# Kernel optimization log

Hardware: AMD Instinct MI355X
Metric: run time of the kernel (lower is better)

The kernel has to match this reference:

```python
import jax, jax.numpy as jnp
import numpy as np

DIM = 768
HEADS = 12
HD = DIM // HEADS
SCALE = HD ** -0.5


def setup_inputs() -> dict:
    key = jax.random.key(0)
    ks = jax.random.split(key, 12)
    B, N = 2, 2048
    s = DIM ** -0.5
    return {
        "x1": jax.random.normal(ks[0], (B, N, DIM), jnp.float32),
        "x2": jax.random.normal(ks[1], (B, N, DIM), jnp.float32),
        "Wq": jax.random.normal(ks[2], (DIM, DIM), jnp.float32) * s,
        "bq": jax.random.normal(ks[3], (DIM,), jnp.float32) * 0.01,
        "Wk": jax.random.normal(ks[4], (DIM, DIM), jnp.float32) * s,
        "bk": jax.random.normal(ks[5], (DIM,), jnp.float32) * 0.01,
        "Wv": jax.random.normal(ks[6], (DIM, DIM), jnp.float32) * s,
        "bv": jax.random.normal(ks[7], (DIM,), jnp.float32) * 0.01,
        "Wo": jax.random.normal(ks[8], (DIM, DIM), jnp.float32) * s,
        "bo": jax.random.normal(ks[9], (DIM,), jnp.float32) * 0.01,
        "cross_scale": jnp.array([0.5], jnp.float32),
    }


def _heads(x, W, b):
    # torch Linear: x @ W.T + b; then (B,N,H,hd) -> (B,H,N,hd)
    B, N, _ = x.shape
    y = x @ W.T + b
    return y.reshape(B, N, HEADS, HD).transpose(0, 2, 1, 3)


def reference(x1, x2, Wq, bq, Wk, bk, Wv, bv, Wo, bo, cross_scale):
    B, N, C = x1.shape
    q1, k1, v1 = _heads(x1, Wq, bq), _heads(x1, Wk, bk), _heads(x1, Wv, bv)
    q2, k2, v2 = _heads(x2, Wq, bq), _heads(x2, Wk, bk), _heads(x2, Wv, bv)

    s = cross_scale[0]
    attn11 = jnp.einsum('bhqd,bhkd->bhqk', q1, k1) * SCALE
    attn22 = jnp.einsum('bhqd,bhkd->bhqk', q2, k2) * SCALE
    attn12 = jnp.einsum('bhqd,bhkd->bhqk', q1, k2) * SCALE
    attn21 = jnp.einsum('bhqd,bhkd->bhqk', q2, k1) * SCALE

    a1 = jax.nn.softmax((1.0 - s) * attn11 + s * attn12, axis=-1)
    a2 = jax.nn.softmax((1.0 - s) * attn22 + s * attn21, axis=-1)

    o1 = jnp.einsum('bhqk,bhkd->bhqd', a1, v1).transpose(0, 2, 1, 3).reshape(B, N, C)
    o2 = jnp.einsum('bhqk,bhkd->bhqd', a2, v2).transpose(0, 2, 1, 3).reshape(B, N, C)

    out1 = o1 @ Wo.T + bo
    out2 = o2 @ Wo.T + bo
    return out1, out2
```

## Files before the change

kernel.cpp:

```cpp
#include <hip/hip_runtime.h>

#define KDIM 768
#define HALF 3145728
#define XAELEMS 6291456
#define WELEMS 589824
#define QS 0.18033688f

typedef __attribute__((ext_vector_type(8))) short short8;
typedef __attribute__((ext_vector_type(4))) short short4_;
typedef __attribute__((ext_vector_type(4))) float float4_;
typedef __attribute__((ext_vector_type(2))) unsigned int uint2_;

__device__ __forceinline__ unsigned short f2bf(float f) {
  unsigned int u = __float_as_uint(f);
  u += 0x7fffu + ((u >> 16) & 1u);
  return (unsigned short)(u >> 16);
}

__device__ __forceinline__ unsigned int pack2bf(float a, float b) {
  unsigned int ua = __float_as_uint(a) + 0x8000u;
  unsigned int ub = __float_as_uint(b) + 0x8000u;
  return __builtin_amdgcn_perm(ub, ua, 0x07060302);
}

__device__ __forceinline__ void gll16(const void* g, void* l) {
  __builtin_amdgcn_global_load_lds(
      (const __attribute__((address_space(1))) unsigned int*)g,
      (__attribute__((address_space(3))) unsigned int*)l, 16, 0, 0);
}

__global__ void prep_x_kernel(const float* __restrict__ x1, const float* __restrict__ x2,
                              const float* __restrict__ cs,
                              unsigned short* __restrict__ xa, unsigned short* __restrict__ xb) {
  const int i = (blockIdx.x * 256 + threadIdx.x) * 4;
  const float s = cs[0], t_ = 1.0f - s;
  float4 a = *(const float4*)(x1 + i);
  float4 b = *(const float4*)(x2 + i);
  ushort4 ua = { f2bf(a.x), f2bf(a.y), f2bf(a.z), f2bf(a.w) };
  ushort4 ub = { f2bf(b.x), f2bf(b.y), f2bf(b.z), f2bf(b.w) };
  *(ushort4*)(xa + i) = ua;
  *(ushort4*)(xa + HALF + i) = ub;
  ushort4 c1 = { f2bf(t_*a.x + s*b.x), f2bf(t_*a.y + s*b.y), f2bf(t_*a.z + s*b.z), f2bf(t_*a.w + s*b.w) };
  ushort4 c2 = { f2bf(t_*b.x + s*a.x), f2bf(t_*b.y + s*a.y), f2bf(t_*b.z + s*a.z), f2bf(t_*b.w + s*a.w) };
  *(ushort4*)(xb + i) = c1;
  *(ushort4*)(xb + HALF + i) = c2;
}

__global__ void conv_w4_kernel(const float* __restrict__ w0, const float* __restrict__ w1,
                               const float* __restrict__ w2, const float* __restrict__ w3,
                               unsigned short* __restrict__ o0, unsigned short* __restrict__ o1,
                               unsigned short* __restrict__ o2, unsigned short* __restrict__ o3) {
  const int z = blockIdx.y;
  const float* w = (z == 0) ? w0 : (z == 1) ? w1 : (z == 2) ? w2 : w3;
  unsigned short* o = (z == 0) ? o0 : (z == 1) ? o1 : (z == 2) ? o2 : o3;
  const int i = (blockIdx.x * 256 + threadIdx.x) * 4;
  float4 a = *(const float4*)(w + i);
  ushort4 ua = { f2bf(a.x), f2bf(a.y), f2bf(a.z), f2bf(a.w) };
  *(ushort4*)(o + i) = ua;
}

__device__ __forceinline__ void gemm_mainloop(const unsigned short* __restrict__ A,
                                              const unsigned short* __restrict__ W,
                                              unsigned short* As, unsigned short* Bs,
                                              int m0, int n0, int t, float4_ (&acc)[4][4]) {
  const int lane = t & 63, quad = lane >> 4, lrow = lane & 15;
  const int wave = t >> 6;
  const int wm = (wave & 1) * 64, wn = (wave >> 1) * 64;
  for (int kt = 0; kt < KDIM; kt += 64) {
#pragma unroll
    for (int i = 0; i < 4; i++) {
      const int li = i * 256 + t;
      const int row = li >> 3, cc = (li & 7) * 8;
      gll16(A + (size_t)(m0 + row) * KDIM + kt + cc, As + li * 8);
      gll16(W + (size_t)(n0 + row) * KDIM + kt + cc, Bs + li * 8);
    }
    __syncthreads();
#pragma unroll
    for (int kk = 0; kk < 2; kk++) {
      short8 af[4], bfr[4];
#pragma unroll
      for (int i = 0; i < 4; i++)
        af[i] = *(const short8*)(As + (wm + i * 16 + lrow) * 64 + kk * 32 + quad * 8);
#pragma unroll
      for (int j = 0; j < 4; j++)
        bfr[j] = *(const short8*)(Bs + (wn + j * 16 + lrow) * 64 + kk * 32 + quad * 8);
#pragma unroll
      for (int i = 0; i < 4; i++)
#pragma unroll
        for (int j = 0; j < 4; j++)
          acc[i][j] = __builtin_amdgcn_mfma_f32_16x16x32_bf16(af[i], bfr[j], acc[i][j], 0, 0, 0);
    }
    __syncthreads();
  }
}

__global__ __launch_bounds__(256, 2)
void qkv_gemm(const unsigned short* __restrict__ xa, const unsigned short* __restrict__ xb,
              const unsigned short* __restrict__ wq, const unsigned short* __restrict__ wk,
              const unsigned short* __restrict__ wv,
              const float* __restrict__ bq, const float* __restrict__ bk, const float* __restrict__ bv,
              unsigned short* __restrict__ qo, unsigned short* __restrict__ ko,
              unsigned short* __restrict__ vto) {
  __shared__ __align__(16) unsigned short smem[16384];
  unsigned short* As = smem;
  unsigned short* Bs = smem + 8192;
  const int t = threadIdx.x;
  const int z = blockIdx.z;
  const int m0 = blockIdx.x * 128, n0 = blockIdx.y * 128;
  const unsigned short* A = (z == 1) ? xb : xa;
  const unsigned short* W = (z == 0) ? wq : (z == 1) ? wk : wv;
  const float* bias = (z == 0) ? bq : (z == 1) ? bk : bv;
  float4_ acc[4][4];
#pragma unroll
  for (int i = 0; i < 4; i++)
#pragma unroll
    for (int j = 0; j < 4; j++) acc[i][j] = (float4_){0.f, 0.f, 0.f, 0.f};
  gemm_mainloop(A, W, As, Bs, m0, n0, t, acc);

  const int lane = t & 63, quad = lane >> 4, lrow = lane & 15;
  const int wave = t >> 6;
  const int wm = (wave & 1) * 64, wn = (wave >> 1) * 64;

  if (z == 2) {
    unsigned short* Tb = smem + wave * 4096;
#pragma unroll
    for (int i = 0; i < 4; i++) {
#pragma unroll
      for (int j = 0; j < 4; j++) {
        const int nl = j * 16 + lrow;
        const float bn = bias[n0 + wn + nl];
#pragma unroll
        for (int r = 0; r < 4; r++) {
          const int ml = i * 16 + quad * 4 + r;
          const int c = ml >> 3;
          Tb[nl * 64 + ((c ^ (nl & 7)) * 8) + (ml & 7)] = f2bf(acc[i][j][r] + bn);
        }
      }
    }
    __asm__ __volatile__("s_waitcnt lgkmcnt(0)");
    const int sb = (m0 + wm) >> 11;
    const int hh = (n0 + wn) >> 6;
    const int tokbase = ((m0 + wm) & 2047);
#pragma unroll
    for (int i3 = 0; i3 < 8; i3++) {
      const int ci = i3 * 64 + lane;
      const int row = ci >> 3, p = ci & 7;
      short8 rd = *(const short8*)(Tb + row * 64 + p * 8);
      const int c = p ^ (row & 7);
      *(short8*)(vto + ((size_t)(sb * 12 + hh) * 64 + row) * 2048 + tokbase + c * 8) = rd;
    }
  } else {
    unsigned short* dst = (z == 0) ? qo : ko;
    const float scale = (z == 0) ? QS : 1.0f;
#pragma unroll
    for (int i = 0; i < 4; i++) {
#pragma unroll
      for (int j = 0; j < 4; j++) {
        const int n = n0 + wn + j * 16 + lrow;
        const float bn = bias[n];
#pragma unroll
        for (int r = 0; r < 4; r++) {
          const int m = m0 + wm + i * 16 + quad * 4 + r;
          dst[(size_t)m * KDIM + n] = f2bf((acc[i][j][r] + bn) * scale);
        }
      }
    }
  }
}

__global__ __launch_bounds__(256, 2)
void out_gemm(const unsigned short* __restrict__ ob, const unsigned short* __restrict__ wo,
              const float* __restrict__ bo, float* __restrict__ out) {
  __shared__ __align__(16) unsigned short As[128 * 64];
  __shared__ __align__(16) unsigned short Bs[128 * 64];
  const int t = threadIdx.x;
  const int m0 = blockIdx.x * 128, n0 = blockIdx.y * 128;
  float4_ acc[4][4];
#pragma unroll
  for (int i = 0; i < 4; i++)
#pragma unroll
    for (int j = 0; j < 4; j++) acc[i][j] = (float4_){0.f, 0.f, 0.f, 0.f};
  gemm_mainloop(ob, wo, As, Bs, m0, n0, t, acc);

  const int lane = t & 63, quad = lane >> 4, lrow = lane & 15;
  const int wave = t >> 6;
  const int wm = (wave & 1) * 64, wn = (wave >> 1) * 64;
#pragma unroll
  for (int i = 0; i < 4; i++) {
#pragma unroll
    for (int j = 0; j < 4; j++) {
      const int n = n0 + wn + j * 16 + lrow;
      const float bn = bo[n];
#pragma unroll
      for (int r = 0; r < 4; r++) {
        const int m = m0 + wm + i * 16 + quad * 4 + r;
        out[(size_t)m * KDIM + n] = acc[i][j][r] + bn;
      }
    }
  }
}

__global__ __launch_bounds__(256, 2)
void attn_kernel(const unsigned short* __restrict__ qg, const unsigned short* __restrict__ kg,
                 const unsigned short* __restrict__ vt, unsigned short* __restrict__ o) {
  __shared__ __align__(16) unsigned short Ks[3][64 * 64];
  __shared__ __align__(16) unsigned short Vs[3][64 * 64];
  const int prob = blockIdx.x % 48;
  const int q0 = (blockIdx.x / 48) * 128;
  const int sb = prob / 12, h = prob % 12;
  const int t = threadIdx.x, w = t >> 6, lane = t & 63, quad = lane >> 4, lrow = lane & 15;
  const int mbase = sb * 2048;
  const size_t vbase = (size_t)prob * (64 * 2048);

  short8 bq[2][2];
#pragma unroll
  for (int i = 0; i < 2; i++) {
    const unsigned short* qp = qg + (size_t)(mbase + q0 + w * 32 + i * 16 + lrow) * KDIM + h * 64 + quad * 8;
    bq[i][0] = *(const short8*)qp;
    bq[i][1] = *(const short8*)(qp + 32);
  }
  float l_part[2] = {0.f, 0.f};
  float4_ oa[2][4];
#pragma unroll
  for (int i = 0; i < 2; i++)
#pragma unroll
    for (int d = 0; d < 4; d++) oa[i][d] = (float4_){0.f, 0.f, 0.f, 0.f};

  auto stage = [&](int k0, int b) {
#pragma unroll
    for (int i2 = 0; i2 < 2; i2++) {
      const int li = i2 * 256 + t;
      const int row = li >> 3, p = li & 7;
      const int c = p ^ (row & 7);
      gll16(kg + (size_t)(mbase + k0 + row) * KDIM + h * 64 + c * 8, &Ks[b][li * 8]);
    }
#pragma unroll
    for (int i2 = 0; i2 < 2; i2++) {
      const int li = i2 * 256 + t;
      const int row = li >> 3, p = li & 7;
      const int c = p ^ (row & 7);
      gll16(vt + vbase + (size_t)row * 2048 + k0 + c * 8, &Vs[b][li * 8]);
    }
  };

  auto compute = [&](int b) {
    float4_ st[4][2];
#pragma unroll
    for (int nt = 0; nt < 4; nt++)
#pragma unroll
      for (int i = 0; i < 2; i++) st[nt][i] = (float4_){0.f, 0.f, 0.f, 0.f};
#pragma unroll
    for (int kk = 0; kk < 2; kk++) {
#pragma unroll
      for (int nt = 0; nt < 4; nt++) {
        short8 ak = *(const short8*)(&Ks[b][(nt * 16 + lrow) * 64 + (((kk * 4 + quad) ^ (lrow & 7)) * 8)]);
        st[nt][0] = __builtin_amdgcn_mfma_f32_16x16x32_bf16(ak, bq[0][kk], st[nt][0], 0, 0, 0);
        st[nt][1] = __builtin_amdgcn_mfma_f32_16x16x32_bf16(ak, bq[1][kk], st[nt][1], 0, 0, 0);
      }
    }

    short4_ pb[2][4];
#pragma unroll
    for (int nt = 0; nt < 4; nt++)
#pragma unroll
      for (int i = 0; i < 2; i++) {
        const float p0 = __builtin_amdgcn_exp2f(st[nt][i][0]);
        const float p1 = __builtin_amdgcn_exp2f(st[nt][i][1]);
        const float p2 = __builtin_amdgcn_exp2f(st[nt][i][2]);
        const float p3 = __builtin_amdgcn_exp2f(st[nt][i][3]);
        l_part[i] += (p0 + p1) + (p2 + p3);
        uint2_ uu = { pack2bf(p0, p1), pack2bf(p2, p3) };
        pb[i][nt] = __builtin_bit_cast(short4_, uu);
      }

#pragma unroll
    for (int g = 0; g < 2; g++) {
      const int cp0 = (((g * 4 + (quad >> 1)) ^ (lrow & 7)) * 8) + (quad & 1) * 4;
      const int cp1 = (((g * 4 + 2 + (quad >> 1)) ^ (lrow & 7)) * 8) + (quad & 1) * 4;
      const short8 b80 = __builtin_shufflevector(pb[0][2 * g], pb[0][2 * g + 1], 0, 1, 2, 3, 4, 5, 6, 7);
      const short8 b81 = __builtin_shufflevector(pb[1][2 * g], pb[1][2 * g + 1], 0, 1, 2, 3, 4, 5, 6, 7);
#pragma unroll
      for (int dt = 0; dt < 4; dt++) {
        const int rb = (dt * 16 + lrow) * 64;
        short4_ av0 = *(const short4_*)(&Vs[b][rb + cp0]);
        short4_ av1 = *(const short4_*)(&Vs[b][rb + cp1]);
        short8 a8 = __builtin_shufflevector(av0, av1, 0, 1, 2, 3, 4, 5, 6, 7);
        oa[0][dt] = __builtin_amdgcn_mfma_f32_16x16x32_bf16(a8, b80, oa[0][dt], 0, 0, 0);
        oa[1][dt] = __builtin_amdgcn_mfma_f32_16x16x32_bf16(a8, b81, oa[1][dt], 0, 0, 0);
      }
    }
  };

  stage(0, 0);
  stage(64, 1);

#define STEP(KT, CUR, STG)                                   \
  do {                                                       \
    asm volatile("s_waitcnt vmcnt(4)" ::: "memory");         \
    __builtin_amdgcn_s_barrier();                            \
    __builtin_amdgcn_sched_barrier(0);                       \
    stage(((KT) + 2) * 64, (STG));                           \
    compute(CUR);                                            \
  } while (0)

  for (int kt0 = 0; kt0 < 30; kt0 += 3) {
    STEP(kt0, 0, 2);
    STEP(kt0 + 1, 1, 0);
    STEP(kt0 + 2, 2, 1);
  }
  asm volatile("s_waitcnt vmcnt(4)" ::: "memory");
  __builtin_amdgcn_s_barrier();
  __builtin_amdgcn_sched_barrier(0);
  compute(0);
  asm volatile("s_waitcnt vmcnt(0)" ::: "memory");
  __builtin_amdgcn_s_barrier();
  __builtin_amdgcn_sched_barrier(0);
  compute(1);
#undef STEP

#pragma unroll
  for (int i = 0; i < 2; i++) {
    float l = l_part[i];
    l += __shfl_xor(l, 16);
    l += __shfl_xor(l, 32);
    const float inv = 1.0f / l;
    const size_t m = (size_t)mbase + q0 + w * 32 + i * 16 + lrow;
#pragma unroll
    for (int dt = 0; dt < 4; dt++) {
      uint2_ uu = { pack2bf(oa[i][dt][0] * inv, oa[i][dt][1] * inv),
                    pack2bf(oa[i][dt][2] * inv, oa[i][dt][3] * inv) };
      *(uint2_*)(o + m * KDIM + h * 64 + dt * 16 + quad * 4) = uu;
    }
  }
}

extern "C" void kernel_launch(void* const* d_in, const int* in_sizes, int n_in,
                              void* d_out, int out_size, void* d_ws, size_t ws_size,
                              hipStream_t stream) {
  const float* x1 = (const float*)d_in[0];
  const float* x2 = (const float*)d_in[1];
  const float* Wq = (const float*)d_in[2];
  const float* bq = (const float*)d_in[3];
  const float* Wk = (const float*)d_in[4];
  const float* bk = (const float*)d_in[5];
  const float* Wv = (const float*)d_in[6];
  const float* bv = (const float*)d_in[7];
  const float* Wo = (const float*)d_in[8];
  const float* bo = (const float*)d_in[9];
  const float* cs = (const float*)d_in[10];
  float* out = (float*)d_out;

  char* ws = (char*)d_ws;
  size_t off = 0;
  auto alloc = [&](size_t bytes) {
    void* p = ws + off;
    off += (bytes + 255) & ~(size_t)255;
    return p;
  };
  unsigned short* xa  = (unsigned short*)alloc((size_t)XAELEMS * 2);
  unsigned short* xb  = (unsigned short*)alloc((size_t)XAELEMS * 2);
  unsigned short* wqb = (unsigned short*)alloc((size_t)WELEMS * 2);
  unsigned short* wkb = (unsigned short*)alloc((size_t)WELEMS * 2);
  unsigned short* wvb = (unsigned short*)alloc((size_t)WELEMS * 2);
  unsigned short* wob = (unsigned short*)alloc((size_t)WELEMS * 2);
  unsigned short* qg  = (unsigned short*)alloc((size_t)XAELEMS * 2);
  unsigned short* kgb = (unsigned short*)alloc((size_t)XAELEMS * 2);
  unsigned short* vtb = (unsigned short*)alloc((size_t)XAELEMS * 2);
  unsigned short* ob  = (unsigned short*)alloc((size_t)XAELEMS * 2);

  prep_x_kernel<<<HALF / 1024, 256, 0, stream>>>(x1, x2, cs, xa, xb);
  conv_w4_kernel<<<dim3(WELEMS / 1024, 4), 256, 0, stream>>>(Wq, Wk, Wv, Wo, wqb, wkb, wvb, wob);
  qkv_gemm<<<dim3(64, 6, 3), 256, 0, stream>>>(xa, xb, wqb, wkb, wvb, bq, bk, bv, qg, kgb, vtb);
  attn_kernel<<<48 * 16, 256, 0, stream>>>(qg, kgb, vtb, ob);
  out_gemm<<<dim3(64, 6), 256, 0, stream>>>(ob, wob, bo, out);
}
```

Measured before the change: 224.2 us.

## Compute softmax row sums via MFMA with ones and pre-permute V layout

The attention kernel now gets the softmax denominator from an extra MFMA against an all-ones bf16 vector instead of scalar adds plus cross-lane shuffles. It also switches P to truncating bf16 packing, which keeps the numerator and the MFMA-computed denominator consistent. The V-transpose writer in the projection kernel now stores tokens pre-permuted, so the attention loop can read one 16-byte LDS vector instead of two 8-byte reads and a shuffle. The cost is two extra MFMAs per group in exchange for fewer VALU ops and LDS instructions, and the epilogue now does two half-width LDS reads.

Result: faster. 215.6 us (-3.8%).

```diff
diff --git a/kernel.cpp b/kernel.cpp
--- a/kernel.cpp
+++ b/kernel.cpp
@@ -21,6 +21,10 @@
   unsigned int ua = __float_as_uint(a) + 0x8000u;
   unsigned int ub = __float_as_uint(b) + 0x8000u;
   return __builtin_amdgcn_perm(ub, ua, 0x07060302);
+}
+
+__device__ __forceinline__ unsigned int pack2bf_t(float a, float b) {
+  return __builtin_amdgcn_perm(__float_as_uint(b), __float_as_uint(a), 0x07060302);
 }
 
 __device__ __forceinline__ void gll16(const void* g, void* l) {
@@ -144,10 +148,15 @@
 #pragma unroll
     for (int i3 = 0; i3 < 8; i3++) {
       const int ci = i3 * 64 + lane;
-      const int row = ci >> 3, p = ci & 7;
-      short8 rd = *(const short8*)(Tb + row * 64 + p * 8);
-      const int c = p ^ (row & 7);
-      *(short8*)(vto + ((size_t)(sb * 12 + hh) * 64 + row) * 2048 + tokbase + c * 8) = rd;
+      const int row = ci >> 3, cp_ = ci & 7;
+      const int bl = (cp_ >> 2) * 4 + ((cp_ & 3) >> 1);
+      const int off = (cp_ & 1) * 4;
+      const int chlo = bl ^ (row & 7);
+      const int chhi = (bl + 2) ^ (row & 7);
+      short4_ lo = *(const short4_*)(Tb + row * 64 + chlo * 8 + off);
+      short4_ hi = *(const short4_*)(Tb + row * 64 + chhi * 8 + off);
+      short8 rd = __builtin_shufflevector(lo, hi, 0, 1, 2, 3, 4, 5, 6, 7);
+      *(short8*)(vto + ((size_t)(sb * 12 + hh) * 64 + row) * 2048 + tokbase + cp_ * 8) = rd;
     }
   } else {
     unsigned short* dst = (z == 0) ? qo : ko;
@@ -212,6 +221,10 @@
   const int mbase = sb * 2048;
   const size_t vbase = (size_t)prob * (64 * 2048);
 
+  short8 ones8;
+#pragma unroll
+  for (int zz = 0; zz < 8; zz++) ones8[zz] = (short)0x3F80;
+
   short8 bq[2][2];
 #pragma unroll
   for (int i = 0; i < 2; i++) {
@@ -219,12 +232,14 @@
     bq[i][0] = *(const short8*)qp;
     bq[i][1] = *(const short8*)(qp + 32);
   }
-  float l_part[2] = {0.f, 0.f};
+  float4_ la[2];
   float4_ oa[2][4];
 #pragma unroll
-  for (int i = 0; i < 2; i++)
+  for (int i = 0; i < 2; i++) {
+    la[i] = (float4_){0.f, 0.f, 0.f, 0.f};
 #pragma unroll
     for (int d = 0; d < 4; d++) oa[i][d] = (float4_){0.f, 0.f, 0.f, 0.f};
+  }
 
   auto stage = [&](int k0, int b) {
 #pragma unroll
@@ -268,23 +283,20 @@
         const float p1 = __builtin_amdgcn_exp2f(st[nt][i][1]);
         const float p2 = __builtin_amdgcn_exp2f(st[nt][i][2]);
         const float p3 = __builtin_amdgcn_exp2f(st[nt][i][3]);
-        l_part[i] += (p0 + p1) + (p2 + p3);
-        uint2_ uu = { pack2bf(p0, p1), pack2bf(p2, p3) };
+        uint2_ uu = { pack2bf_t(p0, p1), pack2bf_t(p2, p3) };
         pb[i][nt] = __builtin_bit_cast(short4_, uu);
       }
 
 #pragma unroll
     for (int g = 0; g < 2; g++) {
-      const int cp0 = (((g * 4 + (quad >> 1)) ^ (lrow & 7)) * 8) + (quad & 1) * 4;
-      const int cp1 = (((g * 4 + 2 + (quad >> 1)) ^ (lrow & 7)) * 8) + (quad & 1) * 4;
       const short8 b80 = __builtin_shufflevector(pb[0][2 * g], pb[0][2 * g + 1], 0, 1, 2, 3, 4, 5, 6, 7);
       const short8 b81 = __builtin_shufflevector(pb[1][2 * g], pb[1][2 * g + 1], 0, 1, 2, 3, 4, 5, 6, 7);
+      la[0] = __builtin_amdgcn_mfma_f32_16x16x32_bf16(ones8, b80, la[0], 0, 0, 0);
+      la[1] = __builtin_amdgcn_mfma_f32_16x16x32_bf16(ones8, b81, la[1], 0, 0, 0);
 #pragma unroll
       for (int dt = 0; dt < 4; dt++) {
-        const int rb = (dt * 16 + lrow) * 64;
-        short4_ av0 = *(const short4_*)(&Vs[b][rb + cp0]);
-        short4_ av1 = *(const short4_*)(&Vs[b][rb + cp1]);
-        short8 a8 = __builtin_shufflevector(av0, av1, 0, 1, 2, 3, 4, 5, 6, 7);
+        const int rb = (dt * 16 + lrow) * 64 + (((g * 4 + quad) ^ (lrow & 7)) * 8);
+        short8 a8 = *(const short8*)(&Vs[b][rb]);
         oa[0][dt] = __builtin_amdgcn_mfma_f32_16x16x32_bf16(a8, b80, oa[0][dt], 0, 0, 0);
         oa[1][dt] = __builtin_amdgcn_mfma_f32_16x16x32_bf16(a8, b81, oa[1][dt], 0, 0, 0);
       }
@@ -320,10 +332,7 @@
 
 #pragma unroll
   for (int i = 0; i < 2; i++) {
-    float l = l_part[i];
-    l += __shfl_xor(l, 16);
-    l += __shfl_xor(l, 32);
-    const float inv = 1.0f / l;
+    const float inv = 1.0f / la[i][0];
     const size_t m = (size_t)mbase + q0 + w * 32 + i * 16 + lrow;
 #pragma unroll
     for (int dt = 0; dt < 4; dt++) {
```

## Pre-permute V^T token layout so attention loads V with single 16-byte reads

Applied to the files above, without the earlier changes.

The projection kernel now writes V^T with token columns permuted, so each lane's eight P·V operands are contiguous. The attention kernel can then fetch V fragments with one 16-byte LDS read instead of two 8-byte reads and a shuffle. The QK^T loop is also reordered to interleave each tile's exp/pack with the next tile's MFMAs, and to defer the last tile's exp past the first P·V group, so MFMA and VALU work overlap. This relies on the producer and consumer permutations matching exactly; the projection store now needs two 8-byte LDS reads per chunk.

Result: slower. 235.5 us (+5.1%).

```diff
diff --git a/kernel.cpp b/kernel.cpp
--- a/kernel.cpp
+++ b/kernel.cpp
@@ -144,10 +144,15 @@
 #pragma unroll
     for (int i3 = 0; i3 < 8; i3++) {
       const int ci = i3 * 64 + lane;
-      const int row = ci >> 3, p = ci & 7;
-      short8 rd = *(const short8*)(Tb + row * 64 + p * 8);
-      const int c = p ^ (row & 7);
-      *(short8*)(vto + ((size_t)(sb * 12 + hh) * 64 + row) * 2048 + tokbase + c * 8) = rd;
+      const int row = ci >> 3, cp_ = ci & 7;
+      const int bl = (cp_ >> 2) * 4 + ((cp_ & 3) >> 1);
+      const int off = (cp_ & 1) * 4;
+      const int chlo = bl ^ (row & 7);
+      const int chhi = (bl + 2) ^ (row & 7);
+      short4_ lo = *(const short4_*)(Tb + row * 64 + chlo * 8 + off);
+      short4_ hi = *(const short4_*)(Tb + row * 64 + chhi * 8 + off);
+      short8 rd = __builtin_shufflevector(lo, hi, 0, 1, 2, 3, 4, 5, 6, 7);
+      *(short8*)(vto + ((size_t)(sb * 12 + hh) * 64 + row) * 2048 + tokbase + cp_ * 8) = rd;
     }
   } else {
     unsigned short* dst = (z == 0) ? qo : ko;
@@ -212,6 +217,8 @@
   const int mbase = sb * 2048;
   const size_t vbase = (size_t)prob * (64 * 2048);
 
+  const float4_ z4 = (float4_){0.f, 0.f, 0.f, 0.f};
+
   short8 bq[2][2];
 #pragma unroll
   for (int i = 0; i < 2; i++) {
@@ -245,49 +252,45 @@
 
   auto compute = [&](int b) {
     float4_ st[4][2];
-#pragma unroll
-    for (int nt = 0; nt < 4; nt++)
-#pragma unroll
-      for (int i = 0; i < 2; i++) st[nt][i] = (float4_){0.f, 0.f, 0.f, 0.f};
-#pragma unroll
-    for (int kk = 0; kk < 2; kk++) {
-#pragma unroll
-      for (int nt = 0; nt < 4; nt++) {
-        short8 ak = *(const short8*)(&Ks[b][(nt * 16 + lrow) * 64 + (((kk * 4 + quad) ^ (lrow & 7)) * 8)]);
-        st[nt][0] = __builtin_amdgcn_mfma_f32_16x16x32_bf16(ak, bq[0][kk], st[nt][0], 0, 0, 0);
-        st[nt][1] = __builtin_amdgcn_mfma_f32_16x16x32_bf16(ak, bq[1][kk], st[nt][1], 0, 0, 0);
-      }
-    }
-
     short4_ pb[2][4];
-#pragma unroll
-    for (int nt = 0; nt < 4; nt++)
+
+    auto exppack = [&](int p) {
 #pragma unroll
       for (int i = 0; i < 2; i++) {
-        const float p0 = __builtin_amdgcn_exp2f(st[nt][i][0]);
-        const float p1 = __builtin_amdgcn_exp2f(st[nt][i][1]);
-        const float p2 = __builtin_amdgcn_exp2f(st[nt][i][2]);
-        const float p3 = __builtin_amdgcn_exp2f(st[nt][i][3]);
+        const float p0 = __builtin_amdgcn_exp2f(st[p][i][0]);
+        const float p1 = __builtin_amdgcn_exp2f(st[p][i][1]);
+        const float p2 = __builtin_amdgcn_exp2f(st[p][i][2]);
+        const float p3 = __builtin_amdgcn_exp2f(st[p][i][3]);
         l_part[i] += (p0 + p1) + (p2 + p3);
         uint2_ uu = { pack2bf(p0, p1), pack2bf(p2, p3) };
-        pb[i][nt] = __builtin_bit_cast(short4_, uu);
-      }
+        pb[i][p] = __builtin_bit_cast(short4_, uu);
+      }
+    };
+
+#pragma unroll
+    for (int nt = 0; nt < 4; nt++) {
+      const int rowb = (nt * 16 + lrow) * 64;
+      short8 ak0 = *(const short8*)(&Ks[b][rowb + ((quad ^ (lrow & 7)) * 8)]);
+      short8 ak1 = *(const short8*)(&Ks[b][rowb + (((4 + quad) ^ (lrow & 7)) * 8)]);
+      st[nt][0] = __builtin_amdgcn_mfma_f32_16x16x32_bf16(ak0, bq[0][0], z4, 0, 0, 0);
+      st[nt][1] = __builtin_amdgcn_mfma_f32_16x16x32_bf16(ak0, bq[1][0], z4, 0, 0, 0);
+      st[nt][0] = __builtin_amdgcn_mfma_f32_16x16x32_bf16(ak1, bq[0][1], st[nt][0], 0, 0, 0);
+      st[nt][1] = __builtin_amdgcn_mfma_f32_16x16x32_bf16(ak1, bq[1][1], st[nt][1], 0, 0, 0);
+      if (nt >= 1) exppack(nt - 1);
+    }
 
 #pragma unroll
     for (int g = 0; g < 2; g++) {
-      const int cp0 = (((g * 4 + (quad >> 1)) ^ (lrow & 7)) * 8) + (quad & 1) * 4;
-      const int cp1 = (((g * 4 + 2 + (quad >> 1)) ^ (lrow & 7)) * 8) + (quad & 1) * 4;
       const short8 b80 = __builtin_shufflevector(pb[0][2 * g], pb[0][2 * g + 1], 0, 1, 2, 3, 4, 5, 6, 7);
       const short8 b81 = __builtin_shufflevector(pb[1][2 * g], pb[1][2 * g + 1], 0, 1, 2, 3, 4, 5, 6, 7);
 #pragma unroll
       for (int dt = 0; dt < 4; dt++) {
-        const int rb = (dt * 16 + lrow) * 64;
-        short4_ av0 = *(const short4_*)(&Vs[b][rb + cp0]);
-        short4_ av1 = *(const short4_*)(&Vs[b][rb + cp1]);
-        short8 a8 = __builtin_shufflevector(av0, av1, 0, 1, 2, 3, 4, 5, 6, 7);
+        const int rb = (dt * 16 + lrow) * 64 + (((g * 4 + quad) ^ (lrow & 7)) * 8);
+        short8 a8 = *(const short8*)(&Vs[b][rb]);
         oa[0][dt] = __builtin_amdgcn_mfma_f32_16x16x32_bf16(a8, b80, oa[0][dt], 0, 0, 0);
         oa[1][dt] = __builtin_amdgcn_mfma_f32_16x16x32_bf16(a8, b81, oa[1][dt], 0, 0, 0);
       }
+      if (g == 0) exppack(3);
     }
   };
 
```
